# Optimization experiments

Measured on AMD Instinct MI355X. Metric: run time of the kernel, lower is better.

The kernel has to match this reference:

```python
import jax, jax.numpy as jnp
import numpy as np

# Dims from LiftSplatShootGPN defaults
B, N, D, FH, FW, C = 8, 6, 41, 8, 22, 64
OGFH, OGFW = 128, 352
DX = jnp.array([0.5, 0.5, 20.0], dtype=jnp.float32)        # gen_dx_bx
BX = jnp.array([-49.75, -49.75, 0.0], dtype=jnp.float32)
NX = (200, 200, 1)


def _frustum():
    # D x fH x fW x 3, matches create_frustum
    ds = jnp.broadcast_to(jnp.arange(4.0, 45.0, 1.0, dtype=jnp.float32).reshape(D, 1, 1), (D, FH, FW))
    xs = jnp.broadcast_to(jnp.linspace(0.0, OGFW - 1.0, FW, dtype=jnp.float32).reshape(1, 1, FW), (D, FH, FW))
    ys = jnp.broadcast_to(jnp.linspace(0.0, OGFH - 1.0, FH, dtype=jnp.float32).reshape(1, FH, 1), (D, FH, FW))
    return jnp.stack((xs, ys, ds), -1)


def setup_inputs() -> dict:
    key = jax.random.key(0)
    k1, k2, k3, k4, k5, k6 = jax.random.split(key, 6)
    eye = jnp.eye(3, dtype=jnp.float32)
    x_feats = jax.random.normal(k1, (B, N, D, FH, FW, C), dtype=jnp.float32)
    # well-conditioned camera extrinsics / intrinsics
    rots = eye + 0.1 * jax.random.normal(k2, (B, N, 3, 3), dtype=jnp.float32)
    trans = 2.0 * jax.random.normal(k3, (B, N, 3), dtype=jnp.float32)
    intr_base = jnp.array([[278.0, 0.0, 176.0], [0.0, 278.0, 64.0], [0.0, 0.0, 1.0]], dtype=jnp.float32)
    intrins = intr_base + 0.5 * jax.random.normal(k4, (B, N, 3, 3), dtype=jnp.float32) * jnp.array([[1, 0, 1], [0, 1, 1], [0, 0, 0]], dtype=jnp.float32)
    post_rots = eye + 0.01 * jax.random.normal(k5, (B, N, 3, 3), dtype=jnp.float32)
    post_trans = 0.5 * jax.random.normal(k6, (B, N, 3), dtype=jnp.float32)
    return {"x_feats": x_feats, "rots": rots, "trans": trans, "intrins": intrins,
            "post_rots": post_rots, "post_trans": post_trans}


def _forward(x_feats, rots, trans, intrins, post_rots, post_trans):
    frustum = _frustum()  # [D,FH,FW,3]
    # get_geometry: undo image-space augmentation
    pts = frustum[None, None] - post_trans[:, :, None, None, None, :]            # [B,N,D,H,W,3]
    inv_pr = jnp.linalg.inv(post_rots)                                           # [B,N,3,3]
    pts = jnp.einsum('bnij,bndhwj->bndhwi', inv_pr, pts)
    # unproject: (u*d, v*d, d)
    pts = jnp.concatenate((pts[..., :2] * pts[..., 2:3], pts[..., 2:3]), axis=-1)
    combine = jnp.einsum('bnij,bnjk->bnik', rots, jnp.linalg.inv(intrins))
    geom = jnp.einsum('bnij,bndhwj->bndhwi', combine, pts) + trans[:, :, None, None, None, :]

    # voxel_pooling
    Nprime = B * N * D * FH * FW
    x = x_feats.reshape(Nprime, C)
    # torch .long() truncates toward zero -> astype(int32) matches
    g = ((geom - (BX - DX / 2.0)) / DX).reshape(Nprime, 3).astype(jnp.int32)
    bix = jnp.repeat(jnp.arange(B, dtype=jnp.int32), Nprime // B)
    kept = ((g[:, 0] >= 0) & (g[:, 0] < NX[0]) &
            (g[:, 1] >= 0) & (g[:, 1] < NX[1]) &
            (g[:, 2] >= 0) & (g[:, 2] < NX[2]))
    # QuickCumsum computes per-voxel segment sums; scatter-add of all kept points
    # into the dense grid yields identical values without the sort.
    flat = ((bix * NX[2] + g[:, 2]) * NX[0] + g[:, 0]) * NX[1] + g[:, 1]
    flat = jnp.where(kept, flat, 0)
    xm = jnp.where(kept[:, None], x, jnp.zeros((), x.dtype))
    grid = jnp.zeros((B * NX[2] * NX[0] * NX[1], C), dtype=x.dtype).at[flat].add(xm)
    # final: [B, C, nz, nx0, nx1] -> cat over nz (nz=1) -> [B, C, 200, 200]
    grid = grid.reshape(B, NX[2], NX[0], NX[1], C)
    final = jnp.transpose(grid, (0, 1, 4, 2, 3)).reshape(B, NX[2] * C, NX[0], NX[1])
    return final


def reference(x_feats, rots, trans, intrins, post_rots, post_trans):
    return _forward(x_feats, rots, trans, intrins, post_rots, post_trans)
```

## Files before the change

kernel.cpp:

```cpp
#include <hip/hip_runtime.h>

#define B_   8
#define N_   6
#define D_   41
#define FH_  8
#define FW_  22
#define C_   64
#define NPRIME (B_*N_*D_*FH_*FW_)
#define NBLK_PTS 1353
#define PTS_PER_CAM (D_*FH_*FW_)
#define NX0  200
#define NX1  200
#define G1H  2
#define NB2  (B_ * NX0 * G1H)
#define OUTSZ (B_*C_*NX0*NX1)
#define RROWS 16
#define NGRP ((NX0 + RROWS - 1) / RROWS)

__device__ void lapack_inv3_f32(const float Ain[9], float Aout[9]) {
    #pragma clang fp contract(off)
    float a[9];
    for (int r = 0; r < 3; ++r)
        for (int c = 0; c < 3; ++c)
            a[c*3 + r] = Ain[r*3 + c];
    int ipiv[3];
    for (int j = 0; j < 3; ++j) {
        int p = j;
        float amax = fabsf(a[j*3 + j]);
        for (int i = j + 1; i < 3; ++i) {
            float v = fabsf(a[j*3 + i]);
            if (v > amax) { amax = v; p = i; }
        }
        ipiv[j] = p;
        if (p != j)
            for (int c = 0; c < 3; ++c) { float t = a[c*3+j]; a[c*3+j] = a[c*3+p]; a[c*3+p] = t; }
        float d = 1.0f / a[j*3 + j];
        for (int i = j + 1; i < 3; ++i) a[j*3 + i] = a[j*3 + i] * d;
        for (int jj = j + 1; jj < 3; ++jj) {
            float temp = -a[jj*3 + j];
            for (int ii = j + 1; ii < 3; ++ii)
                a[jj*3 + ii] = a[jj*3 + ii] + a[j*3 + ii] * temp;
        }
    }
    for (int j = 0; j < 3; ++j) {
        float ajj_inv = 1.0f / a[j*3 + j];
        a[j*3 + j] = ajj_inv;
        float AJJ = -ajj_inv;
        for (int jj = 0; jj < j; ++jj) {
            float temp = a[j*3 + jj];
            for (int i = 0; i < jj; ++i)
                a[j*3 + i] = a[j*3 + i] + temp * a[jj*3 + i];
            a[j*3 + jj] = a[j*3 + jj] * a[jj*3 + jj];
        }
        for (int i = 0; i < j; ++i) a[j*3 + i] = a[j*3 + i] * AJJ;
    }
    float work[3];
    for (int j = 2; j >= 0; --j) {
        for (int i = j + 1; i < 3; ++i) { work[i] = a[j*3 + i]; a[j*3 + i] = 0.0f; }
        for (int jj = j + 1; jj < 3; ++jj) {
            float temp = -work[jj];
            for (int i = 0; i < 3; ++i)
                a[j*3 + i] = a[j*3 + i] + temp * a[jj*3 + i];
        }
    }
    for (int j = 2; j >= 0; --j) {
        int p = ipiv[j];
        if (p != j)
            for (int i = 0; i < 3; ++i) { float t = a[j*3+i]; a[j*3+i] = a[p*3+i]; a[p*3+i] = t; }
    }
    for (int r = 0; r < 3; ++r)
        for (int c = 0; c < 3; ++c)
            Aout[r*3 + c] = a[c*3 + r];
}

__global__ void prep_kernel(const float* __restrict__ rots,
                            const float* __restrict__ trans,
                            const float* __restrict__ intrins,
                            const float* __restrict__ post_rots,
                            const float* __restrict__ post_trans,
                            float* __restrict__ mats,
                            int* __restrict__ counts) {
    #pragma clang fp contract(off)
    int t = threadIdx.x;
    for (int i = t; i < NB2; i += 256) counts[i] = 0;
    if (t >= B_ * N_) return;
    float pr[9], ipr[9], K[9], iK[9];
    for (int i = 0; i < 9; ++i) { pr[i] = post_rots[t*9 + i]; K[i] = intrins[t*9 + i]; }
    lapack_inv3_f32(pr, ipr);
    lapack_inv3_f32(K, iK);
    float* m = mats + t * 24;
    for (int i = 0; i < 9; ++i) m[i] = ipr[i];
    for (int i = 0; i < 3; ++i)
        for (int k = 0; k < 3; ++k) {
            float s = rots[t*9 + i*3 + 0] * iK[0*3 + k];
            s = s + rots[t*9 + i*3 + 1] * iK[1*3 + k];
            s = s + rots[t*9 + i*3 + 2] * iK[2*3 + k];
            m[9 + i*3 + k] = s;
        }
    for (int i = 0; i < 3; ++i) {
        m[18 + i] = post_trans[t*3 + i];
        m[21 + i] = trans[t*3 + i];
    }
}

__global__ void __launch_bounds__(256) geom_kernel(
        const float* __restrict__ mats,
        unsigned int* __restrict__ pcode,
        int* __restrict__ counts) {
    #pragma clang fp contract(off)
    __shared__ unsigned int hist[NB2];
    int t = threadIdx.x;
    int p = blockIdx.x * 256 + t;
    for (int i = t; i < NB2; i += 256) hist[i] = 0u;
    __syncthreads();

    int w  = p % FW_;
    int h  = (p / FW_) % FH_;
    int d  = (p / (FW_ * FH_)) % D_;
    int bn = p / PTS_PER_CAM;
    int b  = bn / N_;

    const float* m = mats + bn * 24;

    float xs = (w == FW_ - 1) ? 351.0f : (float)((double)w * (351.0 / 21.0));
    float ys = (h == FH_ - 1) ? 127.0f : (float)((double)h * (127.0 / 7.0));
    float ds = 4.0f + (float)d;

    float px = xs - m[18], py = ys - m[19], pz = ds - m[20];
    float qx = m[0]*px;  qx = qx + m[1]*py;  qx = qx + m[2]*pz;
    float qy = m[3]*px;  qy = qy + m[4]*py;  qy = qy + m[5]*pz;
    float qz = m[6]*px;  qz = qz + m[7]*py;  qz = qz + m[8]*pz;

    float ux = qx * qz, uy = qy * qz, uz = qz;

    float gx = m[9]*ux;   gx = gx + m[10]*uy;  gx = gx + m[11]*uz;  gx = gx + m[21];
    float gy = m[12]*ux;  gy = gy + m[13]*uy;  gy = gy + m[14]*uz;  gy = gy + m[22];
    float gz = m[15]*ux;  gz = gz + m[16]*uy;  gz = gz + m[17]*uz;  gz = gz + m[23];

    float cx = (gx - (-50.0f)) / 0.5f;
    float cy = (gy - (-50.0f)) / 0.5f;
    float cz = (gz - (-10.0f)) / 20.0f;
    int g0 = (int)cx;
    int g1 = (int)cy;
    int g2 = (int)cz;

    bool kept = (g0 >= 0) && (g0 < NX0) && (g1 >= 0) && (g1 < NX1) && (g2 == 0);
    if (kept) {
        int g1h = g1 / 100;
        int r   = g1 - g1h * 100;
        int bk  = (b * NX0 + g0) * G1H + g1h;
        pcode[p] = ((unsigned int)bk << 7) | (unsigned int)r;
        atomicAdd(&hist[bk], 1u);
    } else {
        pcode[p] = 0xFFFFFFFFu;
    }
    __syncthreads();
    for (int i = t; i < NB2; i += 256) {
        unsigned int hv = hist[i];
        if (hv) atomicAdd(&counts[i], (int)hv);
    }
}

__global__ void scan_kernel(const int* __restrict__ counts,
                            int* __restrict__ offsets,
                            int* __restrict__ cursor) {
    __shared__ int ts[128];
    int t = threadIdx.x;
    const int PER = NB2 / 128;
    int base = t * PER;
    int mysum = 0;
    for (int j = 0; j < PER; ++j) mysum += counts[base + j];
    ts[t] = mysum;
    __syncthreads();
    for (int off = 1; off < 128; off <<= 1) {
        int v = (t >= off) ? ts[t - off] : 0;
        __syncthreads();
        ts[t] += v;
        __syncthreads();
    }
    int run = (t > 0) ? ts[t - 1] : 0;
    for (int j = 0; j < PER; ++j) {
        offsets[base + j] = run;
        cursor[base + j]  = run;
        run += counts[base + j];
    }
    if (t == 127) offsets[NB2] = run;
}

__global__ void __launch_bounds__(256) place_kernel(
        const unsigned int* __restrict__ pcode,
        int* __restrict__ cursor,
        unsigned int* __restrict__ entries) {
    __shared__ int cnt[NB2];
    int t = threadIdx.x;
    int p = blockIdx.x * 256 + t;
    for (int i = t; i < NB2; i += 256) cnt[i] = 0;
    __syncthreads();
    unsigned int code = pcode[p];
    bool kept = (code != 0xFFFFFFFFu);
    int bk = (int)(code >> 7);
    int lr = 0;
    if (kept) lr = atomicAdd(&cnt[bk], 1);
    __syncthreads();
    for (int i = t; i < NB2; i += 256) {
        int c = cnt[i];
        if (c) cnt[i] = atomicAdd(&cursor[i], c);
    }
    __syncthreads();
    if (kept) {
        int r   = (int)(code & 127u);
        int bh  = bk >> 1;
        int g0  = bh % NX0;
        int g1  = (bk & 1) * 100 + r;
        entries[cnt[bk] + lr] = ((unsigned int)(g0 & 15) << 27) |
                                ((unsigned int)g1 << 19) | (unsigned int)p;
    }
}

__global__ void __launch_bounds__(512) render_kernel(
        const float* __restrict__ x_feats,
        const unsigned int* __restrict__ entries,
        const int* __restrict__ offsets,
        float* __restrict__ out) {
    __shared__ float acc[2 * RROWS * NX1];
    const int CHS = RROWS * NX1;
    int blk = blockIdx.x;
    int g   = blk % NGRP;
    int cp  = (blk / NGRP) & 31;
    int b   = blk / (NGRP * 32);
    int c0  = cp * 2;
    int t   = threadIdx.x;
    int row0  = g * RROWS;
    int nrows = (NX0 - row0 < RROWS) ? (NX0 - row0) : RROWS;
    int nf    = nrows * NX1;

    for (int i = t; i < 2 * CHS; i += 512) acc[i] = 0.0f;
    __syncthreads();

    int bk0 = b * (NX0 * G1H) + row0 * G1H;
    int s = offsets[bk0];
    int e = offsets[bk0 + nrows * G1H];
    for (int i = s + t; i < e; i += 512) {
        unsigned int v = entries[i];
        int p  = (int)(v & 0x7FFFFu);
        int g1 = (int)((v >> 19) & 0xFFu);
        int rl = (int)(v >> 27);
        float2 f = *(const float2*)&x_feats[(size_t)p * C_ + c0];
        int a = rl * NX1 + g1;
        atomicAdd(&acc[a], f.x);
        atomicAdd(&acc[CHS + a], f.y);
    }
    __syncthreads();

    size_t pl0 = ((size_t)b * C_ + c0) * (NX0 * NX1) + (size_t)row0 * NX1;
    size_t pl1 = pl0 + (size_t)(NX0 * NX1);
    int nf4 = nf >> 2;
    for (int k = t; k < 2 * nf4; k += 512) {
        int ch = k / nf4, kk = k - ch * nf4;
        float4 v = *(float4*)&acc[ch * CHS + kk * 4];
        *(float4*)&out[(ch ? pl1 : pl0) + (size_t)kk * 4] = v;
    }
}

extern "C" void kernel_launch(void* const* d_in, const int* in_sizes, int n_in,
                              void* d_out, int out_size, void* d_ws, size_t ws_size,
                              hipStream_t stream) {
    const float* x_feats    = (const float*)d_in[0];
    const float* rots       = (const float*)d_in[1];
    const float* trans      = (const float*)d_in[2];
    const float* intrins    = (const float*)d_in[3];
    const float* post_rots  = (const float*)d_in[4];
    const float* post_trans = (const float*)d_in[5];
    float* out = (float*)d_out;

    char* w = (char*)d_ws;
    float*        mats       = (float*)w;         w += 48 * 24 * sizeof(float);
    int*          counts     = (int*)w;           w += NB2 * sizeof(int);
    int*          offsets    = (int*)w;           w += (NB2 + 1) * sizeof(int);
    int*          cursor     = (int*)w;           w += NB2 * sizeof(int);
    unsigned int* pcode      = (unsigned int*)w;  w += NPRIME * sizeof(unsigned int);
    unsigned int* entries    = (unsigned int*)w;  w += NPRIME * sizeof(unsigned int);

    prep_kernel<<<1, 256, 0, stream>>>(rots, trans, intrins, post_rots, post_trans,
                                       mats, counts);
    geom_kernel<<<NBLK_PTS, 256, 0, stream>>>(mats, pcode, counts);
    scan_kernel<<<1, 128, 0, stream>>>(counts, offsets, cursor);
    place_kernel<<<NBLK_PTS, 256, 0, stream>>>(pcode, cursor, entries);
    render_kernel<<<B_ * 32 * NGRP, 512, 0, stream>>>(x_feats, entries, offsets, out);
}
```

Measured before the change: 200.5 us.

## Make render blocks persistent over interleaved 8-row groups with 256 threads

The render kernel now uses 8-row tiles and 256-thread blocks. Each block loops over 5 row groups spaced KINT apart, so the grid shrinks from 8*32*13 to 8*32*5 blocks. The smaller shared-memory accumulator and thread count are meant to raise occupancy and spread load more evenly across CUs. The cost is a serial loop with extra barriers per block, and each block only gets at most 5 rounds of latency hiding.

After: 184.6 us. 7.9% less time.

```diff
diff --git a/kernel.cpp b/kernel.cpp
--- a/kernel.cpp
+++ b/kernel.cpp
@@ -14,8 +14,9 @@
 #define G1H  2
 #define NB2  (B_ * NX0 * G1H)
 #define OUTSZ (B_*C_*NX0*NX1)
-#define RROWS 16
-#define NGRP ((NX0 + RROWS - 1) / RROWS)
+#define RROWS 8
+#define NGRP  25
+#define KINT  5
 
 __device__ void lapack_inv3_f32(const float Ain[9], float Aout[9]) {
     #pragma clang fp contract(off)
@@ -217,7 +218,7 @@
     }
 }
 
-__global__ void __launch_bounds__(512) render_kernel(
+__global__ void __launch_bounds__(256) render_kernel(
         const float* __restrict__ x_feats,
         const unsigned int* __restrict__ entries,
         const int* __restrict__ offsets,
@@ -225,40 +226,42 @@
     __shared__ float acc[2 * RROWS * NX1];
     const int CHS = RROWS * NX1;
     int blk = blockIdx.x;
-    int g   = blk % NGRP;
-    int cp  = (blk / NGRP) & 31;
-    int b   = blk / (NGRP * 32);
+    int k   = blk % KINT;
+    int cp  = (blk / KINT) & 31;
+    int b   = blk / (KINT * 32);
     int c0  = cp * 2;
     int t   = threadIdx.x;
-    int row0  = g * RROWS;
-    int nrows = (NX0 - row0 < RROWS) ? (NX0 - row0) : RROWS;
-    int nf    = nrows * NX1;
-
-    for (int i = t; i < 2 * CHS; i += 512) acc[i] = 0.0f;
-    __syncthreads();
-
-    int bk0 = b * (NX0 * G1H) + row0 * G1H;
-    int s = offsets[bk0];
-    int e = offsets[bk0 + nrows * G1H];
-    for (int i = s + t; i < e; i += 512) {
-        unsigned int v = entries[i];
-        int p  = (int)(v & 0x7FFFFu);
-        int g1 = (int)((v >> 19) & 0xFFu);
-        int rl = (int)(v >> 27);
-        float2 f = *(const float2*)&x_feats[(size_t)p * C_ + c0];
-        int a = rl * NX1 + g1;
-        atomicAdd(&acc[a], f.x);
-        atomicAdd(&acc[CHS + a], f.y);
-    }
-    __syncthreads();
-
-    size_t pl0 = ((size_t)b * C_ + c0) * (NX0 * NX1) + (size_t)row0 * NX1;
-    size_t pl1 = pl0 + (size_t)(NX0 * NX1);
-    int nf4 = nf >> 2;
-    for (int k = t; k < 2 * nf4; k += 512) {
-        int ch = k / nf4, kk = k - ch * nf4;
-        float4 v = *(float4*)&acc[ch * CHS + kk * 4];
-        *(float4*)&out[(ch ? pl1 : pl0) + (size_t)kk * 4] = v;
+
+    for (int g = k; g < NGRP; g += KINT) {
+        int row0 = g * RROWS;
+
+        for (int i = t; i < 2 * CHS; i += 256) acc[i] = 0.0f;
+        __syncthreads();
+
+        int bk0 = b * (NX0 * G1H) + row0 * G1H;
+        int s = offsets[bk0];
+        int e = offsets[bk0 + RROWS * G1H];
+        for (int i = s + t; i < e; i += 256) {
+            unsigned int v = entries[i];
+            int p  = (int)(v & 0x7FFFFu);
+            int g1 = (int)((v >> 19) & 0xFFu);
+            int rl = (int)(v >> 27) & 7;
+            float2 f = *(const float2*)&x_feats[(size_t)p * C_ + c0];
+            int a = rl * NX1 + g1;
+            atomicAdd(&acc[a], f.x);
+            atomicAdd(&acc[CHS + a], f.y);
+        }
+        __syncthreads();
+
+        size_t pl0 = ((size_t)b * C_ + c0) * (NX0 * NX1) + (size_t)row0 * NX1;
+        size_t pl1 = pl0 + (size_t)(NX0 * NX1);
+        const int nf4 = CHS / 4;
+        for (int kk2 = t; kk2 < 2 * nf4; kk2 += 256) {
+            int ch = kk2 / nf4, kk = kk2 - ch * nf4;
+            float4 v4 = *(float4*)&acc[ch * CHS + kk * 4];
+            *(float4*)&out[(ch ? pl1 : pl0) + (size_t)kk * 4] = v4;
+        }
+        __syncthreads();
     }
 }
 
@@ -286,5 +289,5 @@
     geom_kernel<<<NBLK_PTS, 256, 0, stream>>>(mats, pcode, counts);
     scan_kernel<<<1, 128, 0, stream>>>(counts, offsets, cursor);
     place_kernel<<<NBLK_PTS, 256, 0, stream>>>(pcode, cursor, entries);
-    render_kernel<<<B_ * 32 * NGRP, 512, 0, stream>>>(x_feats, entries, offsets, out);
-}
+    render_kernel<<<B_ * 32 * KINT, 256, 0, stream>>>(x_feats, entries, offsets, out);
+}
```
